# Kernel tuning notes

Measured on AMD Instinct MI355X. Metric: run time of the kernel, lower is better.

## Reference

```python
import jax, jax.numpy as jnp
import numpy as np

B, N, D = 8, 2048, 768
K, H, G = 256, 12, 4
DH = D // H          # 64
EPS = 1e-12


def grouped_pointwise(x, w):
    """Grouped Conv1d with kernel_size=1, no bias.
    x: (b, n, d); w: (g, out_per_g, in_per_g) [torch weight (d, d/g, 1) reshaped].
    """
    b, n, d = x.shape
    g = w.shape[0]
    xg = x.reshape(b, n, g, d // g)
    return jnp.einsum('bngi,goi->bngo', xg, w).reshape(b, n, d)


def setup_inputs() -> dict:
    key = jax.random.key(0)
    ks = jax.random.split(key, 8)
    std_conv = 1.0 / np.sqrt(D // G)   # torch conv default ~ U(-sqrt(1/fan_in), ...)
    std_pk = 1.0 / np.sqrt(K)          # init_ uses last dim of (seq_len, k_dim)
    std_lin = 1.0 / np.sqrt(D)
    return {
        'input_embedding': jax.random.normal(ks[0], (B, N, D), jnp.float32),
        'wq': jax.random.uniform(ks[1], (G, D // G, D // G), jnp.float32, -std_conv, std_conv),
        'wk': jax.random.uniform(ks[2], (G, D // G, D // G), jnp.float32, -std_conv, std_conv),
        'project_k': jax.random.uniform(ks[3], (N, K), jnp.float32, -std_pk, std_pk),
        'w_out': jax.random.uniform(ks[4], (D, D), jnp.float32, -std_lin, std_lin),
        'b_out': jax.random.uniform(ks[5], (D,), jnp.float32, -std_lin, std_lin),
        'gamma': jnp.ones((D,), jnp.float32),
        'beta': jnp.zeros((D,), jnp.float32),
    }


def reference(input_embedding, wq, wk, project_k, w_out, b_out, gamma, beta):
    x = input_embedding                       # (b, n, d)
    b, n, d = x.shape

    queries = grouped_pointwise(x, wq)        # (b, n, d)
    k_raw = grouped_pointwise(x, wk)          # (b, n, d)  (key conv)
    k_proj = jnp.einsum('bnd,nk->bkd', k_raw, project_k)   # (b, K, d)

    # Faithful replication of: keys.permute(0,2,1).view(b, K, h, dh)
    # (memory-reinterpreting reshape of the (b, d, K) layout)
    keys = jnp.transpose(k_proj, (0, 2, 1)).reshape(b, K, H, DH)
    keys = jnp.transpose(keys, (0, 2, 1, 3))                # (b, h, K, dh)

    # values also come from the key conv (self.value unused in source forward)
    values = k_proj.reshape(b, K, H, DH).transpose(0, 2, 1, 3)   # (b, h, K, dh)
    q = queries.reshape(b, n, H, DH).transpose(0, 2, 1, 3)       # (b, h, n, dh)

    dots = jnp.einsum('bhnd,bhkd->bhnk', q, keys) / np.sqrt(DH)
    attn = jax.nn.softmax(dots, axis=-1)      # dropout = identity (eval)
    ctx = jnp.einsum('bhnk,bhkd->bhnd', attn, values)
    ctx = ctx.transpose(0, 2, 1, 3).reshape(b, n, d)

    out = ctx @ w_out.T + b_out               # nn.Linear
    y = x + out                               # residual
    mu = jnp.mean(y, axis=-1, keepdims=True)
    var = jnp.mean((y - mu) ** 2, axis=-1, keepdims=True)
    return (y - mu) / jnp.sqrt(var + EPS) * gamma + beta
```

## Files before the change

kernel.cpp:

```cpp
#include <hip/hip_runtime.h>
#include <hip/hip_bf16.h>

typedef short short8 __attribute__((ext_vector_type(8)));
typedef short short4v __attribute__((ext_vector_type(4)));
typedef int i32x4 __attribute__((ext_vector_type(4)));
typedef float f32x4 __attribute__((ext_vector_type(4)));

#define MFMA(a, b, c) __builtin_amdgcn_mfma_f32_16x16x32_bf16((a), (b), (c), 0, 0, 0)

__device__ __forceinline__ short f2bf(float f) {
  unsigned u = __builtin_bit_cast(unsigned, f);
  unsigned r = u + 0x7FFFu + ((u >> 16) & 1u);
  return (short)(r >> 16);
}

__device__ __forceinline__ float bf2f(short s) {
  unsigned u = ((unsigned)(unsigned short)s) << 16;
  return __builtin_bit_cast(float, u);
}

__device__ __forceinline__ short8 cvt8(float4 a, float4 b) {
  short8 t;
  t[0] = f2bf(a.x); t[1] = f2bf(a.y); t[2] = f2bf(a.z); t[3] = f2bf(a.w);
  t[4] = f2bf(b.x); t[5] = f2bf(b.y); t[6] = f2bf(b.z); t[7] = f2bf(b.w);
  return t;
}

__global__ __launch_bounds__(256) void k_prep(
    const float* __restrict__ wq, const float* __restrict__ wk,
    const float* __restrict__ wout, const float* __restrict__ pk,
    short* __restrict__ wqb, short* __restrict__ wkb,
    short* __restrict__ woutb, short* __restrict__ pkT)
{
  int idx = blockIdx.x * 256 + threadIdx.x;
  if (idx < 147456) { wqb[idx] = f2bf(wq[idx]); wkb[idx] = f2bf(wk[idx]); }
  if (idx < 589824) { woutb[idx] = f2bf(wout[idx]); }
  if (idx < 524288) {
    int n = idx >> 8, k = idx & 255;
    pkT[(size_t)k * 2048 + n] = f2bf(pk[idx]);
  }
}

__global__ __launch_bounds__(256, 2) void k_conv(
    const float* __restrict__ x, const short* __restrict__ wqb,
    short* __restrict__ qo, short* __restrict__ xbT)
{
  __shared__ __align__(16) short Xs[64 * 192];
  const int tid = threadIdx.x, lane = tid & 63, w = tid >> 6;
  const int g = blockIdx.y;
  const int m0 = blockIdx.x * 64;
  const int wr = (w >> 1) * 32, wcol = (w & 1) * 96;
  const int lrow = lane & 15, g4 = lane >> 4, lk8 = g4 * 8;

  {
    const int r = tid >> 2, q = tid & 3;
    const int sw = (r ^ (r >> 3)) & 7;
    const float* src = x + (size_t)(m0 + r) * 768 + g * 192;
#pragma unroll
    for (int i = 0; i < 6; i++) {
      const int col = i * 32 + q * 8;
      float4 v0 = *(const float4*)(src + col);
      float4 v1 = *(const float4*)(src + col + 4);
      const int o = col >> 3;
      *(short8*)&Xs[r * 192 + ((o ^ sw) << 3)] = cvt8(v0, v1);
    }
  }
  __syncthreads();

  f32x4 acc[2][6];
#pragma unroll
  for (int mi = 0; mi < 2; mi++)
#pragma unroll
    for (int cf = 0; cf < 6; cf++) acc[mi][cf] = (f32x4)0.f;

  const int row0 = wr + lrow, row1 = wr + 16 + lrow;
  const int sw0 = (row0 ^ (row0 >> 3)) & 7;
  const int sw1 = (row1 ^ (row1 >> 3)) & 7;

#pragma unroll
  for (int s = 0; s < 6; s++) {
    const int k0 = s * 32;
    const int ob = (k0 >> 3) + g4;
    short8 a0 = *(const short8*)&Xs[row0 * 192 + ((ob ^ sw0) << 3)];
    short8 a1 = *(const short8*)&Xs[row1 * 192 + ((ob ^ sw1) << 3)];
#pragma unroll
    for (int cf = 0; cf < 6; cf++) {
      short8 bb = *(const short8*)(wqb + ((size_t)g * 192 + wcol + cf * 16 + lrow) * 192 + k0 + lk8);
      acc[0][cf] = MFMA(a0, bb, acc[0][cf]);
      acc[1][cf] = MFMA(a1, bb, acc[1][cf]);
    }
  }

#pragma unroll
  for (int mi = 0; mi < 2; mi++)
#pragma unroll
    for (int cf = 0; cf < 6; cf++)
#pragma unroll
      for (int j = 0; j < 4; j++) {
        int m = m0 + wr + mi * 16 + g4 * 4 + j;
        qo[(size_t)m * 768 + g * 192 + wcol + cf * 16 + lrow] = f2bf(acc[mi][cf][j]);
      }

  {
    const int b = m0 >> 11, n0 = m0 & 2047;
    const int el = tid >> 3, oct = tid & 7;
#pragma unroll
    for (int ec = 0; ec < 6; ec++) {
      const int c = ec * 32 + el;
      const int o = c >> 3, ci = c & 7;
      short8 v;
#pragma unroll
      for (int u = 0; u < 8; u++) {
        const int n = oct * 8 + u;
        v[u] = Xs[n * 192 + (((o ^ (u ^ oct)) << 3)) + ci];
      }
      *(short8*)(xbT + ((size_t)b * 768 + g * 192 + c) * 2048 + n0 + oct * 8) = v;
    }
  }
}

__global__ __launch_bounds__(512, 4) void k_xproj(
    const short* __restrict__ pkT, const short* __restrict__ xbT,
    float* __restrict__ xproj)
{
  __shared__ __align__(16) short A2[2][64][72];
  __shared__ __align__(16) short B2[2][64][72];
  const int tid = threadIdx.x, lane = tid & 63, w = tid >> 6;
  const int f = blockIdx.x;
  const int xcd = f & 7, rem = f >> 3;
  const int k2t4 = rem & 3, eb8 = rem >> 2;
  const int e_b = eb8 * 8 + xcd;
  const int k2t = k2t4 * 64;
  const int et = (e_b % 12) * 64, b = e_b / 12;
  const int lrow = lane & 15, g4 = lane >> 4, lk8 = g4 * 8;
  const int wa = (w & 3) * 16, wb = (w >> 2) * 32;

  const int r = tid >> 3, c8 = tid & 7;
  const short* aSrc = pkT + (size_t)(k2t + r) * 2048 + c8 * 8;
  const short* bSrc = xbT + ((size_t)b * 768 + et + r) * 2048 + c8 * 8;

  {
    short8 gA = *(const short8*)aSrc;
    short8 gB = *(const short8*)bSrc;
    *(short8*)&A2[0][r][c8 * 8] = gA;
    *(short8*)&B2[0][r][c8 * 8] = gB;
  }
  __syncthreads();

  f32x4 acc[2];
  acc[0] = (f32x4)0.f; acc[1] = (f32x4)0.f;

  short8 gA, gB;
#pragma unroll 2
  for (int t = 0; t < 32; ++t) {
    const int cur = t & 1;
    if (t < 31) {
      gA = *(const short8*)(aSrc + (t + 1) * 64);
      gB = *(const short8*)(bSrc + (t + 1) * 64);
    }
    short8 af0 = *(const short8*)&A2[cur][wa + lrow][lk8];
    short8 af1 = *(const short8*)&A2[cur][wa + lrow][32 + lk8];
    short8 bf00 = *(const short8*)&B2[cur][wb + lrow][lk8];
    short8 bf01 = *(const short8*)&B2[cur][wb + lrow][32 + lk8];
    short8 bf10 = *(const short8*)&B2[cur][wb + 16 + lrow][lk8];
    short8 bf11 = *(const short8*)&B2[cur][wb + 16 + lrow][32 + lk8];
    acc[0] = MFMA(af0, bf00, acc[0]);
    acc[0] = MFMA(af1, bf01, acc[0]);
    acc[1] = MFMA(af0, bf10, acc[1]);
    acc[1] = MFMA(af1, bf11, acc[1]);
    if (t < 31) {
      *(short8*)&A2[cur ^ 1][r][c8 * 8] = gA;
      *(short8*)&B2[cur ^ 1][r][c8 * 8] = gB;
    }
    __syncthreads();
  }

  float* dst = xproj + ((size_t)b * 256 + k2t + wa) * 768 + et + wb;
#pragma unroll
  for (int cf = 0; cf < 2; cf++)
#pragma unroll
    for (int j = 0; j < 4; j++)
      dst[(size_t)(g4 * 4 + j) * 768 + cf * 16 + lrow] = acc[cf][j];
}

__global__ __launch_bounds__(256) void k_kconv(
    float* xpio, const short* __restrict__ wkb)
{
  const int tid = threadIdx.x, lane = tid & 63, w = tid >> 6;
  const int rt = blockIdx.x * 64, g = blockIdx.y, b = blockIdx.z;
  const int wr = (w >> 1) * 32, wcol = (w & 1) * 96;
  const int lrow = lane & 15, g4 = lane >> 4, lk8 = (lane >> 4) * 8;

  f32x4 acc[2][6];
#pragma unroll
  for (int mi = 0; mi < 2; mi++)
#pragma unroll
    for (int cf = 0; cf < 6; cf++) acc[mi][cf] = (f32x4)0.f;

#pragma unroll
  for (int s = 0; s < 6; s++) {
    int k0 = s * 32;
    short8 af[2];
#pragma unroll
    for (int mi = 0; mi < 2; mi++) {
      const float* ap = xpio + ((size_t)b * 256 + rt + wr + mi * 16 + lrow) * 768
                        + g * 192 + k0 + lk8;
      float4 f0 = *(const float4*)ap;
      float4 f1 = *(const float4*)(ap + 4);
      af[mi] = cvt8(f0, f1);
    }
#pragma unroll
    for (int cf = 0; cf < 6; cf++) {
      short8 bb = *(const short8*)(wkb + ((size_t)g * 192 + wcol + cf * 16 + lrow) * 192 + k0 + lk8);
      acc[0][cf] = MFMA(af[0], bb, acc[0][cf]);
      acc[1][cf] = MFMA(af[1], bb, acc[1][cf]);
    }
  }
  __syncthreads();
#pragma unroll
  for (int mi = 0; mi < 2; mi++)
#pragma unroll
    for (int cf = 0; cf < 6; cf++)
#pragma unroll
      for (int j = 0; j < 4; j++) {
        int k2 = rt + wr + mi * 16 + g4 * 4 + j;
        xpio[((size_t)b * 256 + k2) * 768 + g * 192 + wcol + cf * 16 + lrow] =
            acc[mi][cf][j];
      }
}

__global__ __launch_bounds__(256) void k_gather(
    const float* __restrict__ kp, short* __restrict__ Kb, short* __restrict__ Vb)
{
  const int h = blockIdx.x, b = blockIdx.y;
  const int bh = b * 12 + h;
  const int tid = threadIdx.x;
  const float* kpb = kp + (size_t)b * 196608;
  {
    const int kb4 = (h & 3) * 64, doff = h >> 2;
    const int dh = tid & 63, kq = tid >> 6;
    const float* row = kpb + (size_t)(kb4 + dh) * 768 + doff;
    short* dst = Kb + (size_t)bh * 18432 + dh;
#pragma unroll 8
    for (int i = 0; i < 64; i++) {
      int k2 = kq * 64 + i;
      dst[(size_t)k2 * 72] = f2bf(row[3 * k2]);
    }
  }
  {
    short* dst = Vb + (size_t)bh * 16384;
#pragma unroll
    for (int i = 0; i < 8; i++) {
      int oct = tid + 256 * i;
      int k2h = oct >> 6, dh = oct & 63;
      short8 v;
#pragma unroll
      for (int u = 0; u < 8; u++)
        v[u] = f2bf(kpb[(size_t)(k2h * 8 + u) * 768 + h * 64 + dh]);
      *(short8*)&dst[oct * 8] = v;
    }
  }
}

__global__ __launch_bounds__(512, 4) void k_attn(
    const short* __restrict__ qws, const short* __restrict__ Kb,
    const short* __restrict__ Vb, short* __restrict__ ctx)
{
  __shared__ __align__(16) short Kls[18432];
  __shared__ __align__(16) short Vls[16384];
  const int tid = threadIdx.x, lane = tid & 63, w = tid >> 6;
  const int n0 = blockIdx.x * 128;
  const int h = blockIdx.y, b = blockIdx.z;
  const int bh = b * 12 + h;

  {
    const short8* gk = (const short8*)(Kb + (size_t)bh * 18432);
    short8* lk = (short8*)Kls;
#pragma unroll
    for (int i = 0; i < 4; i++) lk[tid + 512 * i] = gk[tid + 512 * i];
    if (tid < 256) lk[tid + 2048] = gk[tid + 2048];
    const short8* gv = (const short8*)(Vb + (size_t)bh * 16384);
    short8* lv = (short8*)Vls;
#pragma unroll
    for (int i = 0; i < 4; i++) lv[tid + 512 * i] = gv[tid + 512 * i];
  }
  const int lrow = lane & 15, g = lane >> 4, lk8 = g * 8;
  const int nrow = n0 + w * 16;
  const short* qp = qws + ((size_t)b * 2048 + nrow + lrow) * 768 + h * 64;
  short8 bq0 = *(const short8*)(qp + lk8);
  short8 bq1 = *(const short8*)(qp + 32 + lk8);
  __syncthreads();

  f32x4 s[16];
#pragma unroll
  for (int fc = 0; fc < 16; fc++) s[fc] = (f32x4)0.f;
  __builtin_amdgcn_s_setprio(1);
#pragma unroll
  for (int fc = 0; fc < 16; fc++) {
    short8 ak0 = *(const short8*)&Kls[(fc * 16 + lrow) * 72 + lk8];
    short8 ak1 = *(const short8*)&Kls[(fc * 16 + lrow) * 72 + 32 + lk8];
    s[fc] = MFMA(ak0, bq0, s[fc]);
    s[fc] = MFMA(ak1, bq1, s[fc]);
  }
  __builtin_amdgcn_s_setprio(0);

  float mx = -3.0e38f;
#pragma unroll
  for (int fc = 0; fc < 16; fc++)
#pragma unroll
    for (int j = 0; j < 4; j++) mx = fmaxf(mx, s[fc][j]);
  mx = fmaxf(mx, __shfl_xor(mx, 16));
  mx = fmaxf(mx, __shfl_xor(mx, 32));
  float sum = 0.f;
#pragma unroll
  for (int fc = 0; fc < 16; fc++)
#pragma unroll
    for (int j = 0; j < 4; j++) {
      float e = __expf(0.125f * (s[fc][j] - mx));
      s[fc][j] = e; sum += e;
    }
  sum += __shfl_xor(sum, 16);
  sum += __shfl_xor(sum, 32);
  float inv = 1.f / sum;

  unsigned pku[16][2];
#pragma unroll
  for (int fc = 0; fc < 16; fc++) {
    pku[fc][0] = (unsigned)(unsigned short)f2bf(s[fc][0] * inv)
               | ((unsigned)(unsigned short)f2bf(s[fc][1] * inv) << 16);
    pku[fc][1] = (unsigned)(unsigned short)f2bf(s[fc][2] * inv)
               | ((unsigned)(unsigned short)f2bf(s[fc][3] * inv) << 16);
  }

  f32x4 o[4];
#pragma unroll
  for (int fd = 0; fd < 4; fd++) o[fd] = (f32x4)0.f;
  const int L0 = ((lane & 16) << 1) + lrow;
  const int L1 = L0 + 16;
  const bool hi = (lane >= 32);
  __builtin_amdgcn_s_setprio(1);
#pragma unroll
  for (int t = 0; t < 8; t++) {
    unsigned a0 = (unsigned)__shfl((int)pku[2 * t][0], L0);
    unsigned a1 = (unsigned)__shfl((int)pku[2 * t][1], L0);
    unsigned a2 = (unsigned)__shfl((int)pku[2 * t][0], L1);
    unsigned a3 = (unsigned)__shfl((int)pku[2 * t][1], L1);
    unsigned c0 = (unsigned)__shfl((int)pku[2 * t + 1][0], L0);
    unsigned c1 = (unsigned)__shfl((int)pku[2 * t + 1][1], L0);
    unsigned c2 = (unsigned)__shfl((int)pku[2 * t + 1][0], L1);
    unsigned c3 = (unsigned)__shfl((int)pku[2 * t + 1][1], L1);
    i32x4 bi = { (int)(hi ? c0 : a0), (int)(hi ? c1 : a1),
                 (int)(hi ? c2 : a2), (int)(hi ? c3 : a3) };
    short8 bfrag = __builtin_bit_cast(short8, bi);
#pragma unroll
    for (int fd = 0; fd < 4; fd++) {
      short8 av = *(const short8*)&Vls[((t * 4 + g) * 64 + fd * 16 + lrow) * 8];
      o[fd] = MFMA(av, bfrag, o[fd]);
    }
  }
  __builtin_amdgcn_s_setprio(0);
#pragma unroll
  for (int fd = 0; fd < 4; fd++) {
    short4v st;
#pragma unroll
    for (int j = 0; j < 4; j++) st[j] = f2bf(o[fd][j]);
    *(short4v*)&ctx[((size_t)b * 2048 + n0 + w * 16 + lrow) * 768
                    + h * 64 + fd * 16 + 4 * g] = st;
  }
}

__global__ __launch_bounds__(512, 4) void k_gemm_y(
    const short* __restrict__ ctx, const short* __restrict__ woutb,
    const float* __restrict__ bout, const float* __restrict__ x,
    short* __restrict__ ybf)
{
  __shared__ __align__(16) short As[2][128][40];
  __shared__ __align__(16) short Bs[2][128][40];
  const int tid = threadIdx.x, lane = tid & 63, w = tid >> 6;
  const int f = blockIdx.x;
  const int xcd = f & 7, rem = f >> 3;
  const int mi_l = rem / 6, ni = rem % 6;
  const int m0 = (xcd * 16 + mi_l) * 128;
  const int n0 = ni * 128;
  const int lrow = lane & 15, g4 = lane >> 4, lk8 = g4 * 8;
  const int wr2 = (w >> 2) * 64, wc4 = (w & 3) * 32;

  const int r = tid >> 2, c8 = (tid & 3) * 8;
  const short* aSrc = ctx + (size_t)(m0 + r) * 768 + c8;
  const short* bSrc = woutb + (size_t)(n0 + r) * 768 + c8;

  {
    short8 gA = *(const short8*)aSrc;
    short8 gB = *(const short8*)bSrc;
    *(short8*)&As[0][r][c8] = gA;
    *(short8*)&Bs[0][r][c8] = gB;
  }
  __syncthreads();

  f32x4 acc[4][2];
#pragma unroll
  for (int rf = 0; rf < 4; rf++)
#pragma unroll
    for (int cf = 0; cf < 2; cf++) acc[rf][cf] = (f32x4)0.f;

  short8 gA, gB;
#pragma unroll 2
  for (int t = 0; t < 24; ++t) {
    const int cur = t & 1;
    if (t < 23) {
      gA = *(const short8*)(aSrc + (t + 1) * 32);
      gB = *(const short8*)(bSrc + (t + 1) * 32);
    }
    short8 af[4], bf[2];
#pragma unroll
    for (int rf = 0; rf < 4; rf++)
      af[rf] = *(const short8*)&As[cur][wr2 + rf * 16 + lrow][lk8];
#pragma unroll
    for (int cf = 0; cf < 2; cf++)
      bf[cf] = *(const short8*)&Bs[cur][wc4 + cf * 16 + lrow][lk8];
#pragma unroll
    for (int cf = 0; cf < 2; cf++)
#pragma unroll
      for (int rf = 0; rf < 4; rf++)
        acc[rf][cf] = MFMA(af[rf], bf[cf], acc[rf][cf]);
    if (t < 23) {
      *(short8*)&As[cur ^ 1][r][c8] = gA;
      *(short8*)&Bs[cur ^ 1][r][c8] = gB;
    }
    __syncthreads();
  }

  float cB[2];
#pragma unroll
  for (int cf = 0; cf < 2; cf++) cB[cf] = bout[n0 + wc4 + cf * 16 + lrow];
#pragma unroll
  for (int rf = 0; rf < 4; rf++)
#pragma unroll
    for (int j = 0; j < 4; j++) {
      int row = m0 + wr2 + rf * 16 + g4 * 4 + j;
      const float* xr = x + (size_t)row * 768 + n0 + wc4;
      short* yr = ybf + (size_t)row * 768 + n0 + wc4;
#pragma unroll
      for (int cf = 0; cf < 2; cf++)
        yr[cf * 16 + lrow] = f2bf(acc[rf][cf][j] + cB[cf] + xr[cf * 16 + lrow]);
    }
}

__global__ __launch_bounds__(256) void k_ln(
    const short* __restrict__ ybf, const float* __restrict__ gamma,
    const float* __restrict__ beta, float* __restrict__ out)
{
  const int tid = threadIdx.x, lane = tid & 63, w = tid >> 6;
  const int half = lane >> 5, l5 = lane & 31;
  const int row = blockIdx.x * 8 + w * 2 + half;
  const short* yr = ybf + (size_t)row * 768;

  float v[24];
  float s1 = 0.f, s2 = 0.f;
#pragma unroll
  for (int j = 0; j < 3; j++) {
    short8 p = *(const short8*)(yr + (l5 + 32 * j) * 8);
#pragma unroll
    for (int u = 0; u < 8; u++) {
      float fv = bf2f(p[u]);
      v[j * 8 + u] = fv;
      s1 += fv; s2 += fv * fv;
    }
  }
  s1 += __shfl_xor(s1, 1, 32);  s2 += __shfl_xor(s2, 1, 32);
  s1 += __shfl_xor(s1, 2, 32);  s2 += __shfl_xor(s2, 2, 32);
  s1 += __shfl_xor(s1, 4, 32);  s2 += __shfl_xor(s2, 4, 32);
  s1 += __shfl_xor(s1, 8, 32);  s2 += __shfl_xor(s2, 8, 32);
  s1 += __shfl_xor(s1, 16, 32); s2 += __shfl_xor(s2, 16, 32);
  float mean = s1 * (1.f / 768.f);
  float var = s2 * (1.f / 768.f) - mean * mean;
  float rstd = rsqrtf(var + 1e-12f);

  float* orow = out + (size_t)row * 768;
#pragma unroll
  for (int j = 0; j < 3; j++) {
    int c0 = (l5 + 32 * j) * 8;
    float4 o0, o1;
    o0.x = (v[j*8+0] - mean) * rstd * gamma[c0+0] + beta[c0+0];
    o0.y = (v[j*8+1] - mean) * rstd * gamma[c0+1] + beta[c0+1];
    o0.z = (v[j*8+2] - mean) * rstd * gamma[c0+2] + beta[c0+2];
    o0.w = (v[j*8+3] - mean) * rstd * gamma[c0+3] + beta[c0+3];
    o1.x = (v[j*8+4] - mean) * rstd * gamma[c0+4] + beta[c0+4];
    o1.y = (v[j*8+5] - mean) * rstd * gamma[c0+5] + beta[c0+5];
    o1.z = (v[j*8+6] - mean) * rstd * gamma[c0+6] + beta[c0+6];
    o1.w = (v[j*8+7] - mean) * rstd * gamma[c0+7] + beta[c0+7];
    *(float4*)(orow + c0) = o0;
    *(float4*)(orow + c0 + 4) = o1;
  }
}

extern "C" void kernel_launch(void* const* d_in, const int* in_sizes, int n_in,
                              void* d_out, int out_size, void* d_ws, size_t ws_size,
                              hipStream_t stream)
{
  const float* x     = (const float*)d_in[0];
  const float* wq    = (const float*)d_in[1];
  const float* wk    = (const float*)d_in[2];
  const float* pk    = (const float*)d_in[3];
  const float* wout  = (const float*)d_in[4];
  const float* bout  = (const float*)d_in[5];
  const float* gamma = (const float*)d_in[6];
  const float* beta  = (const float*)d_in[7];
  float* out = (float*)d_out;

  char* ws = (char*)d_ws;
  short* qbf   = (short*)(ws + 0);
  short* xbT   = (short*)(ws + 25165824);
  float* kpbuf = (float*)(ws + 50331648);
  short* wqb   = (short*)(ws + 56623104);
  short* wkb   = (short*)(ws + 56918016);
  short* woutb = (short*)(ws + 57212928);
  short* pkT   = (short*)(ws + 58392576);
  if (ws_size < 59441152) return;
  short* ctx = (short*)xbT;
  short* ybf = qbf;

  short* Kb = (short*)d_out;
  short* Vb = Kb + 96 * 18432;

  k_prep<<<2304, 256, 0, stream>>>(wq, wk, wout, pk, wqb, wkb, woutb, pkT);
  k_conv<<<dim3(256, 4), 256, 0, stream>>>(x, wqb, qbf, xbT);
  k_xproj<<<384, 512, 0, stream>>>(pkT, xbT, kpbuf);
  k_kconv<<<dim3(4, 4, 8), 256, 0, stream>>>(kpbuf, wkb);
  k_gather<<<dim3(12, 8), 256, 0, stream>>>(kpbuf, Kb, Vb);
  k_attn<<<dim3(16, 12, 8), 512, 0, stream>>>(qbf, Kb, Vb, ctx);
  k_gemm_y<<<768, 512, 0, stream>>>(ctx, woutb, bout, x, ybf);
  k_ln<<<2048, 256, 0, stream>>>(ybf, gamma, beta, out);
}
```

Before: 165.6 us.

## Load fp32 x directly in xproj and drop transposed bf16 staging buffer

Removes the transposed bf16 copy of x that k_conv wrote out (xbT), and instead has k_xproj read fp32 x directly with strided scalar loads, converting to bf16 and storing into an XOR-swizzled LDS tile. This eliminates a 25 MB write and its reread, but the new global loads are scalar, strided by rows and read twice as many bytes (fp32), which may be less coalesced. The swizzle is intended to avoid LDS bank conflicts from the transposed stores.

```diff
diff --git a/kernel.cpp b/kernel.cpp
--- a/kernel.cpp
+++ b/kernel.cpp
@@ -43,7 +43,7 @@
 
 __global__ __launch_bounds__(256, 2) void k_conv(
     const float* __restrict__ x, const short* __restrict__ wqb,
-    short* __restrict__ qo, short* __restrict__ xbT)
+    short* __restrict__ qo)
 {
   __shared__ __align__(16) short Xs[64 * 192];
   const int tid = threadIdx.x, lane = tid & 63, w = tid >> 6;
@@ -100,27 +100,10 @@
         int m = m0 + wr + mi * 16 + g4 * 4 + j;
         qo[(size_t)m * 768 + g * 192 + wcol + cf * 16 + lrow] = f2bf(acc[mi][cf][j]);
       }
-
-  {
-    const int b = m0 >> 11, n0 = m0 & 2047;
-    const int el = tid >> 3, oct = tid & 7;
-#pragma unroll
-    for (int ec = 0; ec < 6; ec++) {
-      const int c = ec * 32 + el;
-      const int o = c >> 3, ci = c & 7;
-      short8 v;
-#pragma unroll
-      for (int u = 0; u < 8; u++) {
-        const int n = oct * 8 + u;
-        v[u] = Xs[n * 192 + (((o ^ (u ^ oct)) << 3)) + ci];
-      }
-      *(short8*)(xbT + ((size_t)b * 768 + g * 192 + c) * 2048 + n0 + oct * 8) = v;
-    }
-  }
 }
 
 __global__ __launch_bounds__(512, 4) void k_xproj(
-    const short* __restrict__ pkT, const short* __restrict__ xbT,
+    const short* __restrict__ pkT, const float* __restrict__ x,
     float* __restrict__ xproj)
 {
   __shared__ __align__(16) short A2[2][64][72];
@@ -137,40 +120,57 @@
 
   const int r = tid >> 3, c8 = tid & 7;
   const short* aSrc = pkT + (size_t)(k2t + r) * 2048 + c8 * 8;
-  const short* bSrc = xbT + ((size_t)b * 768 + et + r) * 2048 + c8 * 8;
+
+  const int se = tid & 63, sn8 = tid >> 6;
+  const int sb8 = (sn8 ^ (se & 7)) * 8;
+  const float* bSrc = x + ((size_t)b * 2048 + sn8 * 8) * 768 + et + se;
 
   {
     short8 gA = *(const short8*)aSrc;
-    short8 gB = *(const short8*)bSrc;
     *(short8*)&A2[0][r][c8 * 8] = gA;
-    *(short8*)&B2[0][r][c8 * 8] = gB;
+    float4 f0, f1;
+    f0.x = bSrc[0 * 768]; f0.y = bSrc[1 * 768];
+    f0.z = bSrc[2 * 768]; f0.w = bSrc[3 * 768];
+    f1.x = bSrc[4 * 768]; f1.y = bSrc[5 * 768];
+    f1.z = bSrc[6 * 768]; f1.w = bSrc[7 * 768];
+    *(short8*)&B2[0][se][sb8] = cvt8(f0, f1);
   }
   __syncthreads();
 
   f32x4 acc[2];
   acc[0] = (f32x4)0.f; acc[1] = (f32x4)0.f;
 
-  short8 gA, gB;
+  const int rB0 = wb + lrow, rB1 = wb + 16 + lrow;
+  const int oB00 = ((g4) ^ (rB0 & 7)) * 8, oB01 = ((4 + g4) ^ (rB0 & 7)) * 8;
+  const int oB10 = ((g4) ^ (rB1 & 7)) * 8, oB11 = ((4 + g4) ^ (rB1 & 7)) * 8;
+
+  short8 gA;
+  float gB[8];
 #pragma unroll 2
   for (int t = 0; t < 32; ++t) {
     const int cur = t & 1;
     if (t < 31) {
       gA = *(const short8*)(aSrc + (t + 1) * 64);
-      gB = *(const short8*)(bSrc + (t + 1) * 64);
+      const float* bs = bSrc + (size_t)(t + 1) * 64 * 768;
+#pragma unroll
+      for (int i = 0; i < 8; i++) gB[i] = bs[i * 768];
     }
     short8 af0 = *(const short8*)&A2[cur][wa + lrow][lk8];
     short8 af1 = *(const short8*)&A2[cur][wa + lrow][32 + lk8];
-    short8 bf00 = *(const short8*)&B2[cur][wb + lrow][lk8];
-    short8 bf01 = *(const short8*)&B2[cur][wb + lrow][32 + lk8];
-    short8 bf10 = *(const short8*)&B2[cur][wb + 16 + lrow][lk8];
-    short8 bf11 = *(const short8*)&B2[cur][wb + 16 + lrow][32 + lk8];
+    short8 bf00 = *(const short8*)&B2[cur][rB0][oB00];
+    short8 bf01 = *(const short8*)&B2[cur][rB0][oB01];
+    short8 bf10 = *(const short8*)&B2[cur][rB1][oB10];
+    short8 bf11 = *(const short8*)&B2[cur][rB1][oB11];
     acc[0] = MFMA(af0, bf00, acc[0]);
     acc[0] = MFMA(af1, bf01, acc[0]);
     acc[1] = MFMA(af0, bf10, acc[1]);
     acc[1] = MFMA(af1, bf11, acc[1]);
     if (t < 31) {
       *(short8*)&A2[cur ^ 1][r][c8 * 8] = gA;
-      *(short8*)&B2[cur ^ 1][r][c8 * 8] = gB;
+      float4 f0, f1;
+      f0.x = gB[0]; f0.y = gB[1]; f0.z = gB[2]; f0.w = gB[3];
+      f1.x = gB[4]; f1.y = gB[5]; f1.z = gB[6]; f1.w = gB[7];
+      *(short8*)&B2[cur ^ 1][se][sb8] = cvt8(f0, f1);
     }
     __syncthreads();
   }
@@ -510,22 +510,21 @@
 
   char* ws = (char*)d_ws;
   short* qbf   = (short*)(ws + 0);
-  short* xbT   = (short*)(ws + 25165824);
+  short* ctx   = (short*)(ws + 25165824);
   float* kpbuf = (float*)(ws + 50331648);
   short* wqb   = (short*)(ws + 56623104);
   short* wkb   = (short*)(ws + 56918016);
   short* woutb = (short*)(ws + 57212928);
   short* pkT   = (short*)(ws + 58392576);
   if (ws_size < 59441152) return;
-  short* ctx = (short*)xbT;
   short* ybf = qbf;
 
   short* Kb = (short*)d_out;
   short* Vb = Kb + 96 * 18432;
 
   k_prep<<<2304, 256, 0, stream>>>(wq, wk, wout, pk, wqb, wkb, woutb, pkT);
-  k_conv<<<dim3(256, 4), 256, 0, stream>>>(x, wqb, qbf, xbT);
-  k_xproj<<<384, 512, 0, stream>>>(pkT, xbT, kpbuf);
+  k_conv<<<dim3(256, 4), 256, 0, stream>>>(x, wqb, qbf);
+  k_xproj<<<384, 512, 0, stream>>>(pkT, x, kpbuf);
   k_kconv<<<dim3(4, 4, 8), 256, 0, stream>>>(kpbuf, wkb);
   k_gather<<<dim3(12, 8), 256, 0, stream>>>(kpbuf, Kb, Vb);
   k_attn<<<dim3(16, 12, 8), 512, 0, stream>>>(qbf, Kb, Vb, ctx);
```

After: 171.9 us. +3.8%, slower.
